# Performance work log

Hardware: AMD Instinct MI355X
Metric: run time of the kernel (lower is better)

Reference implementation:

```python
import jax, jax.numpy as jnp
import numpy as np

NORMALIZED_LENGTH = 1.0
LOSS_WEIGHTS = (0.25, 1.0)
EPS = 1e-12  # matches torch F.normalize eps


def setup_inputs() -> dict:
    key = jax.random.key(0)
    k1, k2 = jax.random.split(key)
    x = jax.random.normal(k1, (16, 128, 64, 64), dtype=jnp.float32)
    codebook = jax.random.normal(k2, (1024, 128), dtype=jnp.float32)
    return {"x": x, "codebook": codebook}


def _forward(x, codebook):
    # --- VQCodebook.forward: normalize x along channel dim (dim=1) ---
    # NOTE: the torch source's codebook renormalization uses non-in-place
    # .div/.mul whose results are discarded, so the codebook is unchanged.
    if NORMALIZED_LENGTH > 0:
        nrm = jnp.linalg.norm(x, axis=1, keepdims=True)  # [B,1,H,W]
        x = NORMALIZED_LENGTH * x / jnp.maximum(nrm, EPS)

    B, C, H, W = x.shape
    z = jnp.transpose(x, (0, 2, 3, 1)).reshape(-1, C)  # [N, C], N = B*H*W

    # Pairwise squared L2 distances via ||z||^2 - 2 z c^T + ||c||^2.
    # argmin of squared distance == argmin of distance.
    z2 = jnp.sum(z * z, axis=1, keepdims=True)             # [N, 1]
    c2 = jnp.sum(codebook * codebook, axis=1)              # [K]
    d2 = z2 - 2.0 * jnp.einsum('nc,kc->nk', z, codebook) + c2[None, :]  # [N, K]
    idx = jnp.argmin(d2, axis=1)                           # [N]

    q = codebook[idx]                                      # [N, C]
    q = q.reshape(B, H, W, C).transpose(0, 3, 1, 2)        # [B, C, H, W]

    lw0, lw1 = LOSS_WEIGHTS
    diff_codebook = jax.lax.stop_gradient(x) - q
    diff_commit = x - jax.lax.stop_gradient(q)
    loss0 = lw0 * jnp.mean(jnp.linalg.norm(diff_codebook, axis=1))
    loss1 = lw1 * jnp.mean(jnp.linalg.norm(diff_commit, axis=1))
    return q, loss0, loss1


def reference(x, codebook):
    return _forward(x, codebook)
```

## Files before the change

### kernel.cpp

```cpp
#include <hip/hip_runtime.h>
#include <math.h>

#define K_CODES 1024
#define C_DIM   128
#define HW      4096
#define CHW     (C_DIM*HW)
#define N_POS   65536
#define Q_ELEMS 8388608

#define WS_S    0
#define WS_C2   256
#define WS_IDX  8192


typedef __attribute__((ext_vector_type(8))) short short8;
typedef __attribute__((ext_vector_type(4))) float f32x4;

__device__ __forceinline__ unsigned short f2bf(float f) {
    unsigned u = __float_as_uint(f);
    u += 0x7FFFu + ((u >> 16) & 1u);
    return (unsigned short)(u >> 16);
}

__device__ __forceinline__ void gll16(const void* g, void* l) {
    __builtin_amdgcn_global_load_lds(
        (const __attribute__((address_space(1))) void*)g,
        (__attribute__((address_space(3))) void*)l, 16, 0, 0);
}

__global__ void prep_kernel(const float* __restrict__ cb, float* __restrict__ ws,
                            unsigned short* __restrict__ cbbf) {
    __shared__ __align__(16) unsigned short srow[128];
    int k = blockIdx.x;
    int l = threadIdx.x;
    if (k == 0 && l == 0) *(float*)((char*)ws + WS_S) = 0.f;
    float v1 = cb[k * C_DIM + l];
    float v2 = cb[k * C_DIM + 64 + l];
    int c1 = l, c2 = 64 + l;
    srow[(((c1 >> 3) ^ (k & 7)) << 3) | (c1 & 7)] = f2bf(v1);
    srow[(((c2 >> 3) ^ (k & 7)) << 3) | (c2 & 7)] = f2bf(v2);
    float ss = v1 * v1 + v2 * v2;
    #pragma unroll
    for (int off = 32; off > 0; off >>= 1) ss += __shfl_down(ss, off);
    if (l == 0) ((float*)((char*)ws + WS_C2))[k] = ss;
    __syncthreads();
    if (l < 16) ((uint4*)cbbf)[k * 16 + l] = ((const uint4*)srow)[l];
}

__global__ __launch_bounds__(256, 2) void vq_mfma(const float* __restrict__ x,
                                                  const float* __restrict__ cb,
                                                  const unsigned short* __restrict__ cbbf,
                                                  const float* __restrict__ c2w,
                                                  int* __restrict__ idxw,
                                                  float* __restrict__ Sw,
                                                  float* __restrict__ out) {
    __shared__ __align__(16) unsigned short cbuf[2][4][4096];
    __shared__ float mbuf[4][4][16][3];
    __shared__ int ibuf[64];

    const int t  = threadIdx.x;
    const int w  = t >> 6;
    const int ln = t & 63;
    const int lp = ln & 15;
    const int q  = ln >> 4;
    const int bid = blockIdx.x;
    const int b   = bid >> 6;
    const int s0  = (bid & 63) << 6;

    const char* gq = (const char*)cbbf + (w << 16);

    {
        const char* gs = gq + (ln << 4);
        char* ld = (char*)&cbuf[0][w][0];
        #pragma unroll
        for (int r = 0; r < 8; ++r) gll16(gs + r * 1024, ld + r * 1024);
    }

    short8 xf[4][4];
    float  r2v[4];
    {
        float ss[4];
        #pragma unroll
        for (int pt = 0; pt < 4; ++pt) {
            ss[pt] = 0.f;
            const float* xgp = x + b * CHW + s0 + pt * 16 + lp;
            #pragma unroll
            for (int cs = 0; cs < 4; ++cs) {
                union { short8 v; unsigned short u[8]; } fu;
                #pragma unroll
                for (int j = 0; j < 8; ++j) {
                    float vv = xgp[(32 * cs + 8 * q + j) * HW];
                    ss[pt] = fmaf(vv, vv, ss[pt]);
                    fu.u[j] = f2bf(vv);
                }
                xf[pt][cs] = fu.v;
            }
        }
        #pragma unroll
        for (int pt = 0; pt < 4; ++pt) {
            float s = ss[pt];
            s += __shfl_xor(s, 16);
            s += __shfl_xor(s, 32);
            r2v[pt] = -2.0f / fmaxf(sqrtf(s), 1e-12f);
        }
    }

    const float FMAX = __uint_as_float(0x7F7FFFFFu);
    float m1[4] = {FMAX, FMAX, FMAX, FMAX};
    float m2[4] = {FMAX, FMAX, FMAX, FMAX};
    float m3[4] = {FMAX, FMAX, FMAX, FMAX};

    asm volatile("s_waitcnt vmcnt(0)" ::: "memory");
    __builtin_amdgcn_sched_barrier(0);

    for (int i = 0; i < 8; ++i) {
        if (i < 7) {
            asm volatile("s_waitcnt lgkmcnt(0)" ::: "memory");
            const char* gs = gq + (i + 1) * 8192 + (ln << 4);
            char* ld = (char*)&cbuf[(i + 1) & 1][w][0];
            #pragma unroll
            for (int r = 0; r < 8; ++r) gll16(gs + r * 1024, ld + r * 1024);
        }

        const int k0 = (w << 8) + (i << 5);
        const unsigned short* cbp = &cbuf[i & 1][w][0];

        f32x4 acc[2][4];
        #pragma unroll
        for (int ct = 0; ct < 2; ++ct)
            #pragma unroll
            for (int pt = 0; pt < 4; ++pt) acc[ct][pt] = 0;

        #pragma unroll
        for (int cs = 0; cs < 4; ++cs) {
            short8 ah[2];
            #pragma unroll
            for (int ct = 0; ct < 2; ++ct) {
                int g = (16 * ct + lp) * 16 + ((4 * cs + q) ^ (lp & 7));
                ah[ct] = *(const short8*)(cbp + g * 8);
            }
            #pragma unroll
            for (int ct = 0; ct < 2; ++ct)
                #pragma unroll
                for (int pt = 0; pt < 4; ++pt)
                    acc[ct][pt] = __builtin_amdgcn_mfma_f32_16x16x32_bf16(
                        ah[ct], xf[pt][cs], acc[ct][pt], 0, 0, 0);
        }

        #pragma unroll
        for (int ct = 0; ct < 2; ++ct) {
            float4 c2vv = *(const float4*)(c2w + k0 + 16 * ct + 4 * q);
            float c2a[4] = {c2vv.x, c2vv.y, c2vv.z, c2vv.w};
            const int kb0 = k0 + 16 * ct + 4 * q;
            #pragma unroll
            for (int pt = 0; pt < 4; ++pt) {
                #pragma unroll
                for (int reg = 0; reg < 4; ++reg) {
                    float s = fmaf(r2v[pt], acc[ct][pt][reg], c2a[reg]);
                    unsigned pb = (__float_as_uint(s) & 0xFFFFFC00u) |
                                  (unsigned)(kb0 + reg);
                    float u  = __uint_as_float(pb);
                    float t3 = __builtin_amdgcn_fmed3f(m2[pt], m3[pt], u);
                    float t2 = __builtin_amdgcn_fmed3f(m1[pt], m2[pt], u);
                    m1[pt] = fminf(m1[pt], u); m2[pt] = t2; m3[pt] = t3;
                }
            }
        }

        if (i < 7) {
            asm volatile("s_waitcnt vmcnt(0)" ::: "memory");
            __builtin_amdgcn_sched_barrier(0);
        }
    }

    #pragma unroll
    for (int d = 16; d <= 32; d <<= 1) {
        #pragma unroll
        for (int pt = 0; pt < 4; ++pt) {
            float o1 = __shfl_xor(m1[pt], d), o2 = __shfl_xor(m2[pt], d),
                  o3 = __shfl_xor(m3[pt], d);
            float u, t2, t3;
            u = o1; t3 = __builtin_amdgcn_fmed3f(m2[pt], m3[pt], u);
            t2 = __builtin_amdgcn_fmed3f(m1[pt], m2[pt], u);
            m1[pt] = fminf(m1[pt], u); m2[pt] = t2; m3[pt] = t3;
            u = o2; t3 = __builtin_amdgcn_fmed3f(m2[pt], m3[pt], u);
            t2 = __builtin_amdgcn_fmed3f(m1[pt], m2[pt], u);
            m1[pt] = fminf(m1[pt], u); m2[pt] = t2; m3[pt] = t3;
            u = o3; t3 = __builtin_amdgcn_fmed3f(m2[pt], m3[pt], u);
            t2 = __builtin_amdgcn_fmed3f(m1[pt], m2[pt], u);
            m1[pt] = fminf(m1[pt], u); m2[pt] = t2; m3[pt] = t3;
        }
    }

    if (ln < 16) {
        #pragma unroll
        for (int pt = 0; pt < 4; ++pt) {
            mbuf[w][pt][lp][0] = m1[pt];
            mbuf[w][pt][lp][1] = m2[pt];
            mbuf[w][pt][lp][2] = m3[pt];
        }
    }
    __syncthreads();

    if (w < 2) {
        float lsum = 0.f;
        #pragma unroll
        for (int ptl = 0; ptl < 2; ++ptl) {
            const int pt = 2 * w + ptl;
            float M1 = FMAX, M2 = FMAX, M3 = FMAX;
            #pragma unroll
            for (int ww = 0; ww < 4; ++ww)
                #pragma unroll
                for (int c = 0; c < 3; ++c) {
                    float u  = mbuf[ww][pt][lp][c];
                    float t3 = __builtin_amdgcn_fmed3f(M2, M3, u);
                    float t2 = __builtin_amdgcn_fmed3f(M1, M2, u);
                    M1 = fminf(M1, u); M2 = t2; M3 = t3;
                }
            int ks[3] = {(int)(__float_as_uint(M1) & 1023u),
                         (int)(__float_as_uint(M2) & 1023u),
                         (int)(__float_as_uint(M3) & 1023u)};

            float xr[32];
            const float* xgp = x + b * CHW + s0 + pt * 16 + lp;
            #pragma unroll
            for (int cs = 0; cs < 4; ++cs)
                #pragma unroll
                for (int j = 0; j < 8; ++j)
                    xr[cs * 8 + j] = xgp[(32 * cs + 8 * q + j) * HW];

            float dots[3];
            #pragma unroll
            for (int jj = 0; jj < 3; ++jj) {
                const float* crow = cb + ks[jj] * C_DIM + 8 * q;
                float p = 0.f;
                #pragma unroll
                for (int cs = 0; cs < 4; ++cs) {
                    float4 a0 = *(const float4*)(crow + 32 * cs);
                    float4 a1 = *(const float4*)(crow + 32 * cs + 4);
                    p = fmaf(xr[cs*8+0], a0.x, p); p = fmaf(xr[cs*8+1], a0.y, p);
                    p = fmaf(xr[cs*8+2], a0.z, p); p = fmaf(xr[cs*8+3], a0.w, p);
                    p = fmaf(xr[cs*8+4], a1.x, p); p = fmaf(xr[cs*8+5], a1.y, p);
                    p = fmaf(xr[cs*8+6], a1.z, p); p = fmaf(xr[cs*8+7], a1.w, p);
                }
                p += __shfl_xor(p, 16);
                p += __shfl_xor(p, 32);
                dots[jj] = p;
            }
            float sb = fmaf(r2v[pt], dots[0], c2w[ks[0]]); int kb = ks[0];
            float s2 = fmaf(r2v[pt], dots[1], c2w[ks[1]]);
            if (s2 < sb || (s2 == sb && ks[1] < kb)) { sb = s2; kb = ks[1]; }
            float s3 = fmaf(r2v[pt], dots[2], c2w[ks[2]]);
            if (s3 < sb || (s3 == sb && ks[2] < kb)) { sb = s3; kb = ks[2]; }

            if (ln < 16) {
                idxw[bid * 64 + pt * 16 + lp] = kb;
                ibuf[pt * 16 + lp] = kb;
            }
            lsum += sqrtf(fmaxf(1.0f + sb, 0.f));
        }
        #pragma unroll
        for (int off = 32; off > 0; off >>= 1) lsum += __shfl_down(lsum, off);
        if (ln == 0) atomicAdd(Sw, 0.25f * lsum);
    }

    __syncthreads();
    if (b != 0) {
        const int row = ibuf[ln];
        const float4* cbr = (const float4*)cb + row * 32;
        float* ob = out + b * CHW + s0 + ln;
        #pragma unroll
        for (int c4 = w * 8; c4 < w * 8 + 8; ++c4) {
            float4 v = cbr[c4];
            float* o = ob + (c4 * 4) * HW;
            o[0]      = v.x;
            o[HW]     = v.y;
            o[2 * HW] = v.z;
            o[3 * HW] = v.w;
        }
    }
}

__global__ void write_q0(const float* __restrict__ cb,
                         const int* __restrict__ idxw,
                         const float* __restrict__ ws,
                         float* __restrict__ out) {
    int id = blockIdx.x * 256 + threadIdx.x;
    int s  = id & 4095;
    int c4 = id >> 12;
    int row = idxw[s];
    float4 v = ((const float4*)cb)[row * 32 + c4];
    float* o = out + (c4 * 4) * HW + s;
    o[0]      = v.x;
    o[HW]     = v.y;
    o[2 * HW] = v.z;
    o[3 * HW] = v.w;
    if (id == 0) {
        float S = *(const float*)((const char*)ws + WS_S);
        float m = S / (float)N_POS;
        out[Q_ELEMS]     = 0.25f * m;
        out[Q_ELEMS + 1] = m;
    }
}

extern "C" void kernel_launch(void* const* d_in, const int* in_sizes, int n_in,
                              void* d_out, int out_size, void* d_ws, size_t ws_size,
                              hipStream_t stream) {
    const float* x  = (const float*)d_in[0];
    const float* cb = (const float*)d_in[1];
    float* out = (float*)d_out;
    float* ws  = (float*)d_ws;

    const float* c2w = (const float*)((const char*)d_ws + WS_C2);
    int*  idxw = (int*)((char*)d_ws + WS_IDX);
    float* Sw  = (float*)((char*)d_ws + WS_S);
    unsigned short* cbbf = (unsigned short*)d_out;

    prep_kernel<<<K_CODES, 64, 0, stream>>>(cb, ws, cbbf);
    vq_mfma    <<<N_POS / 64, 256, 0, stream>>>(x, cb, cbbf, c2w, idxw, Sw, out);
    write_q0   <<<512, 256, 0, stream>>>(cb, idxw, ws, out);
}
```

Baseline: 68.39 us.

## Split x loading across waves and share bf16 tile through LDS

Each wave now loads a distinct quarter of the channels for all 64 positions with coalesced reads, converts to bf16, and stores into a swizzled LDS staging area reusing the second codebook buffer. Partial squared norms are combined through a small shared array, and each wave then reads its MFMA operand fragments from LDS. This removes fourfold redundant global loads of x per block, at the cost of extra LDS traffic and two block barriers before the main loop.

```diff
diff --git a/kernel.cpp b/kernel.cpp
--- a/kernel.cpp
+++ b/kernel.cpp
@@ -56,6 +56,7 @@
                                                   float* __restrict__ out) {
     __shared__ __align__(16) unsigned short cbuf[2][4][4096];
     __shared__ float mbuf[4][4][16][3];
+    __shared__ float nbuf[4][64];
     __shared__ int ibuf[64];
 
     const int t  = threadIdx.x;
@@ -76,34 +77,47 @@
         for (int r = 0; r < 8; ++r) gll16(gs + r * 1024, ld + r * 1024);
     }
 
+    unsigned short* xbuf = &cbuf[1][0][0];
+    {
+        float ssp = 0.f;
+        const float* xgp = x + b * CHW + (w * 32) * HW + s0 + ln;
+        #pragma unroll
+        for (int g = 0; g < 4; ++g) {
+            union { short8 v; unsigned short u[8]; } fu;
+            #pragma unroll
+            for (int j = 0; j < 8; ++j) {
+                float vv = xgp[(g * 8 + j) * HW];
+                ssp = fmaf(vv, vv, ssp);
+                fu.u[j] = f2bf(vv);
+            }
+            int col = (w * 4 + g) ^ (ln & 7);
+            *(short8*)(xbuf + ln * 128 + col * 8) = fu.v;
+        }
+        nbuf[w][ln] = ssp;
+    }
+    __syncthreads();
+
+    float r2v[4];
+    #pragma unroll
+    for (int pt = 0; pt < 4; ++pt) {
+        const int pos = pt * 16 + lp;
+        float s01 = nbuf[0][pos] + nbuf[1][pos];
+        float s23 = nbuf[2][pos] + nbuf[3][pos];
+        float s   = s01 + s23;
+        r2v[pt] = -2.0f / fmaxf(sqrtf(s), 1e-12f);
+    }
+
     short8 xf[4][4];
-    float  r2v[4];
-    {
-        float ss[4];
-        #pragma unroll
-        for (int pt = 0; pt < 4; ++pt) {
-            ss[pt] = 0.f;
-            const float* xgp = x + b * CHW + s0 + pt * 16 + lp;
-            #pragma unroll
-            for (int cs = 0; cs < 4; ++cs) {
-                union { short8 v; unsigned short u[8]; } fu;
-                #pragma unroll
-                for (int j = 0; j < 8; ++j) {
-                    float vv = xgp[(32 * cs + 8 * q + j) * HW];
-                    ss[pt] = fmaf(vv, vv, ss[pt]);
-                    fu.u[j] = f2bf(vv);
-                }
-                xf[pt][cs] = fu.v;
-            }
-        }
-        #pragma unroll
-        for (int pt = 0; pt < 4; ++pt) {
-            float s = ss[pt];
-            s += __shfl_xor(s, 16);
-            s += __shfl_xor(s, 32);
-            r2v[pt] = -2.0f / fmaxf(sqrtf(s), 1e-12f);
-        }
-    }
+    #pragma unroll
+    for (int pt = 0; pt < 4; ++pt)
+        #pragma unroll
+        for (int cs = 0; cs < 4; ++cs) {
+            int col = (4 * cs + q) ^ (lp & 7);
+            xf[pt][cs] = *(const short8*)(xbuf + (pt * 16 + lp) * 128 + col * 8);
+        }
+    asm volatile("s_waitcnt lgkmcnt(0)" ::: "memory");
+    __builtin_amdgcn_sched_barrier(0);
+    __syncthreads();
 
     const float FMAX = __uint_as_float(0x7F7FFFFFu);
     float m1[4] = {FMAX, FMAX, FMAX, FMAX};
```

New measurement: 66.76 us. 1.02x faster.
